# Kernel tuning notes

Hardware: AMD Instinct MI355X
Metric: run time of the kernel (lower is better)

Reference implementation:

```python
import jax, jax.numpy as jnp
import numpy as np

NSITES = 64   # 2 * nphysical spin-orbital sites
BOND = 128    # MPS bond dimension D
BATCH = 16384 # sampled occupation configurations


def setup_inputs() -> dict:
    key = jax.random.key(0)
    k1, k2, k3, k4 = jax.random.split(key, 4)
    # Site tensors A[k, n] in R^{D x D}; scaled so chain products stay O(1).
    data = jax.random.normal(k1, (NSITES, 2, BOND, BOND), dtype=jnp.float32) / jnp.sqrt(jnp.float32(BOND))
    left = jax.random.normal(k2, (BOND,), dtype=jnp.float32)
    right = jax.random.normal(k3, (BOND,), dtype=jnp.float32)
    # Occupation-number vectors (0/1 per spin orbital).
    onstate = jax.random.randint(k4, (BATCH, NSITES), 0, 2, dtype=jnp.int32)
    # Orbital-ordering permutation (identity here).
    image2 = jnp.arange(NSITES, dtype=jnp.int32)
    return {"onstate": onstate, "data": data, "left": left, "right": right, "image2": image2}


def reference(onstate, data, left, right, image2):
    # Reorder physical indices per the stored orbital image: [B, NSITES]
    occ = onstate[:, image2]
    B = occ.shape[0]
    D = left.shape[0]
    v0 = jnp.broadcast_to(left, (B, D))  # left boundary, batched

    def step(v, xs):
        A, n = xs  # A: [2, D, D] site tensor, n: [B] occupations at this site
        # Contract with both quantum-number blocks, then select per sample
        # (equivalent to gathering the block indexed by the occupation).
        v_new = jnp.where((n == 1)[:, None], v @ A[1], v @ A[0])  # [B, D]
        return v_new, None

    vT, _ = jax.lax.scan(step, v0, (data, occ.T))
    return vT @ right  # amplitudes psi(n): [B]
```

## Files before the change

kernel.cpp:

```cpp
#include <hip/hip_runtime.h>
#include <hip/hip_bf16.h>

#define NS 64
#define NP 32
#define DIM 128
#define BATCH_N 16384

typedef float f32x4 __attribute__((ext_vector_type(4)));
typedef _Float16 f16x8 __attribute__((ext_vector_type(8)));
typedef unsigned int u32;
typedef unsigned long long u64;

__device__ __forceinline__ unsigned short f2h(float f) {
    _Float16 h = (_Float16)f;
    return __builtin_bit_cast(unsigned short, h);
}

__global__ __launch_bounds__(256)
void prep_pair_frags(const float* __restrict__ data,
                     unsigned short* __restrict__ afrag) {
    __shared__ float LA[2 * 32 * 129];
    __shared__ float LB[2 * 32 * 128];

    const int p   = blockIdx.x >> 2;
    const int kk  = blockIdx.x & 3;
    const int tid = threadIdx.x;
    const int kgrp = tid >> 5;
    const int mgrp = tid & 31;

    const float* A0 = data + ((size_t)(2 * p) * 2 + 0) * DIM * DIM;
    const float* A1 = A0 + DIM * DIM;
    const float* B0 = data + ((size_t)(2 * p + 1) * 2 + 0) * DIM * DIM;
    const float* B1 = B0 + DIM * DIM;

    for (int c = tid; c < 32 * DIM; c += 256) {
        int kl = c >> 7, j = c & 127;
        float a0 = A0[(kk * 32 + kl) * DIM + j];
        float a1 = A1[(kk * 32 + kl) * DIM + j];
        LA[kl * 129 + j] = a0;
        LA[32 * 129 + kl * 129 + j] = a1 - a0;
    }

    float acc[2][2][4][4];
#pragma unroll
    for (int L = 0; L < 2; ++L)
#pragma unroll
        for (int R = 0; R < 2; ++R)
#pragma unroll
            for (int i = 0; i < 4; ++i)
#pragma unroll
                for (int mi = 0; mi < 4; ++mi) acc[L][R][i][mi] = 0.f;

    for (int ch = 0; ch < 4; ++ch) {
        __syncthreads();
        for (int c = tid; c < 32 * DIM; c += 256) {
            int jl = c >> 7, m = c & 127;
            float b0 = B0[(ch * 32 + jl) * DIM + m];
            float b1 = B1[(ch * 32 + jl) * DIM + m];
            LB[jl * 128 + m] = b0;
            LB[4096 + jl * 128 + m] = b1 - b0;
        }
        __syncthreads();
#pragma unroll 2
        for (int jl = 0; jl < 32; ++jl) {
            int j = ch * 32 + jl;
            float la0[4], la1[4];
#pragma unroll
            for (int i = 0; i < 4; ++i) {
                la0[i] = LA[(kgrp * 4 + i) * 129 + j];
                la1[i] = LA[32 * 129 + (kgrp * 4 + i) * 129 + j];
            }
            f32x4 lb0 = *reinterpret_cast<const f32x4*>(&LB[jl * 128 + mgrp * 4]);
            f32x4 lb1 = *reinterpret_cast<const f32x4*>(&LB[4096 + jl * 128 + mgrp * 4]);
#pragma unroll
            for (int i = 0; i < 4; ++i)
#pragma unroll
                for (int mi = 0; mi < 4; ++mi) {
                    acc[0][0][i][mi] += la0[i] * lb0[mi];
                    acc[1][0][i][mi] += la1[i] * lb0[mi];
                    acc[0][1][i][mi] += la0[i] * lb1[mi];
                    acc[1][1][i][mi] += la1[i] * lb1[mi];
                }
        }
    }

#pragma unroll
    for (int t = 0; t < 4; ++t) {
        int L = t & 1, R = t >> 1;
#pragma unroll
        for (int i = 0; i < 4; ++i)
#pragma unroll
            for (int mi = 0; mi < 4; ++mi) {
                int k = kk * 32 + kgrp * 4 + i;
                int m = mgrp * 4 + mi;
                int g = (k & 31) >> 3, j = k & 7;
                int lane = g * 16 + (m & 15);
                int mm = m >> 4;
                size_t idx =
                    ((((((size_t)p * 4 + t) * 4 + kk) * 8 + mm) * 64 + lane) * 8) + j;
                afrag[idx] = f2h(acc[L][R][i][mi]);
            }
    }
}

__global__ void prep_bits(const int* __restrict__ onstate,
                          const int* __restrict__ image2,
                          u64* __restrict__ bits) {
    int r = blockIdx.x * blockDim.x + threadIdx.x;
    if (r >= BATCH_N) return;
    const int* row = onstate + (size_t)r * NS;
    u64 b = 0;
#pragma unroll 8
    for (int t = 0; t < NS; ++t) {
        b |= ((u64)(row[image2[t]] & 1)) << t;
    }
    bits[r] = b;
}

__global__ __launch_bounds__(512, 2)
void mps_pair(const unsigned short* __restrict__ afrag,
              const u64* __restrict__ occbits,
              const float* __restrict__ left,
              const float* __restrict__ right,
              float* __restrict__ out) {
    __shared__ unsigned short vlds[2][64 * DIM];
    __shared__ float red[64][33];

    const int tid  = threadIdx.x;
    const int wid  = tid >> 6;
    const int lane = tid & 63;
    const int li   = lane & 15;
    const int g    = lane >> 4;
    const int rbase = blockIdx.x * 64;

    u64 bits[4];
#pragma unroll
    for (int rg = 0; rg < 4; ++rg)
        bits[rg] = occbits[rbase + rg * 16 + li];

    u32 rdoff[4][4];
#pragma unroll
    for (int rg = 0; rg < 4; ++rg)
#pragma unroll
        for (int kk = 0; kk < 4; ++kk) {
            int r = rg * 16 + li;
            rdoff[rg][kk] =
                (u32)(r * 256 + kk * 64 + g * 16) ^ ((u32)(r & 7) << 4);
        }
    u32 wroff[4];
#pragma unroll
    for (int rg = 0; rg < 4; ++rg) {
        int r = rg * 16 + li;
        int mbase = wid * 16 + g * 4;
        wroff[rg] = (u32)(r * 256 + mbase * 2) ^ ((u32)(r & 7) << 4);
    }

    for (int c = tid; c < 64 * 16; c += 512) {
        int r  = c >> 4;
        int kc = c & 15;
        unsigned short tmp[8];
#pragma unroll
        for (int j = 0; j < 8; ++j) tmp[j] = f2h(left[kc * 8 + j]);
        u32 byte = (u32)(r * 256 + kc * 16) ^ ((u32)(r & 7) << 4);
        *reinterpret_cast<uint4*>(reinterpret_cast<char*>(&vlds[0][0]) + byte) =
            *reinterpret_cast<uint4*>(tmp);
    }
    __syncthreads();

    const f16x8 zf = {0, 0, 0, 0, 0, 0, 0, 0};

    f16x8 ft[2][4][4];

#define ISSUE(BUF, P_)                                                        \
    {                                                                         \
        const unsigned short* sb_ = afrag + (size_t)(P_) * 65536;             \
        _Pragma("unroll")                                                     \
        for (int t = 0; t < 4; ++t)                                           \
            _Pragma("unroll")                                                 \
            for (int kk = 0; kk < 4; ++kk)                                    \
                ft[BUF][t][kk] = *reinterpret_cast<const f16x8*>(             \
                    sb_ + ((size_t)((t * 4 + kk) * 8 + wid) * 512) +          \
                    lane * 8);                                                \
    }

#define COMPUTE(P_, BUF)                                                      \
    {                                                                         \
        const int p_ = (P_);                                                  \
        const char* vb = reinterpret_cast<const char*>(&vlds[p_ & 1][0]);     \
        char*       wb = reinterpret_cast<char*>(&vlds[(p_ + 1) & 1][0]);     \
        f32x4 acc[4];                                                         \
        _Pragma("unroll")                                                     \
        for (int rg = 0; rg < 4; ++rg) acc[rg] = (f32x4){0.f, 0.f, 0.f, 0.f}; \
        __builtin_amdgcn_s_setprio(1);                                        \
        _Pragma("unroll")                                                     \
        for (int kk = 0; kk < 4; ++kk) {                                      \
            f16x8 bfr[4];                                                     \
            _Pragma("unroll")                                                 \
            for (int rg = 0; rg < 4; ++rg)                                    \
                bfr[rg] =                                                     \
                    *reinterpret_cast<const f16x8*>(vb + rdoff[rg][kk]);      \
            _Pragma("unroll")                                                 \
            for (int rg = 0; rg < 4; ++rg) {                                  \
                bool m0 = (bits[rg] >> (2 * p_)) & 1;                         \
                bool m1 = (bits[rg] >> (2 * p_ + 1)) & 1;                     \
                f16x8 vb0  = m0 ? bfr[rg] : zf;                               \
                f16x8 vb1  = m1 ? bfr[rg] : zf;                               \
                f16x8 vb01 = m1 ? vb0 : zf;                                   \
                acc[rg] = __builtin_amdgcn_mfma_f32_16x16x32_f16(             \
                    ft[BUF][0][kk], bfr[rg], acc[rg], 0, 0, 0);               \
                acc[rg] = __builtin_amdgcn_mfma_f32_16x16x32_f16(             \
                    ft[BUF][1][kk], vb0, acc[rg], 0, 0, 0);                   \
                acc[rg] = __builtin_amdgcn_mfma_f32_16x16x32_f16(             \
                    ft[BUF][2][kk], vb1, acc[rg], 0, 0, 0);                   \
                acc[rg] = __builtin_amdgcn_mfma_f32_16x16x32_f16(             \
                    ft[BUF][3][kk], vb01, acc[rg], 0, 0, 0);                  \
            }                                                                 \
        }                                                                     \
        __builtin_amdgcn_s_setprio(0);                                        \
        if (p_ < NP - 1) {                                                    \
            _Pragma("unroll")                                                 \
            for (int rg = 0; rg < 4; ++rg) {                                  \
                u32 lo = ((u32)f2h(acc[rg][1]) << 16) | f2h(acc[rg][0]);      \
                u32 hi = ((u32)f2h(acc[rg][3]) << 16) | f2h(acc[rg][2]);      \
                uint2 w = {lo, hi};                                           \
                *reinterpret_cast<uint2*>(wb + wroff[rg]) = w;                \
            }                                                                 \
            __syncthreads();                                                  \
        } else {                                                              \
            int mcol = wid * 16 + g * 4;                                      \
            const float4 rv = *reinterpret_cast<const float4*>(right + mcol); \
            _Pragma("unroll")                                                 \
            for (int rg = 0; rg < 4; ++rg) {                                  \
                float pv = acc[rg][0] * rv.x + acc[rg][1] * rv.y +            \
                           acc[rg][2] * rv.z + acc[rg][3] * rv.w;             \
                red[rg * 16 + li][wid * 4 + g] = pv;                          \
            }                                                                 \
            __syncthreads();                                                  \
            if (tid < 64) {                                                   \
                float ssum = 0.f;                                             \
                _Pragma("unroll")                                             \
                for (int i = 0; i < 32; ++i) ssum += red[tid][i];             \
                out[rbase + tid] = ssum;                                      \
            }                                                                 \
        }                                                                     \
    }

    ISSUE(0, 0);
    for (int pp = 0; pp < NP; pp += 2) {
        ISSUE(1, pp + 1);
        COMPUTE(pp, 0);
        if (pp + 2 < NP) ISSUE(0, pp + 2);
        COMPUTE(pp + 1, 1);
    }

#undef ISSUE
#undef COMPUTE
}

extern "C" void kernel_launch(void* const* d_in, const int* in_sizes, int n_in,
                              void* d_out, int out_size, void* d_ws, size_t ws_size,
                              hipStream_t stream) {
    const int*   onstate = (const int*)d_in[0];
    const float* data    = (const float*)d_in[1];
    const float* left    = (const float*)d_in[2];
    const float* right   = (const float*)d_in[3];
    const int*   image2  = (const int*)d_in[4];
    float* out = (float*)d_out;

    unsigned short* afrag = (unsigned short*)d_ws;
    u64* bits = (u64*)((char*)d_ws + (size_t)2097152 * sizeof(unsigned short));

    prep_pair_frags<<<128, 256, 0, stream>>>(data, afrag);
    prep_bits<<<64, 256, 0, stream>>>(onstate, image2, bits);
    mps_pair<<<256, 512, 0, stream>>>(afrag, bits, left, right, out);
}
```

Baseline: 113.4 us.

## Halve rows per block and split fragment prefetch into half-K chunks

The main kernel now processes 32 batch rows per block instead of 64, launching 512 blocks, and raises the occupancy hint from 2 to 4 blocks per CU. The A-fragment register double-buffer is restructured from whole-pair buffers into two half-K chunks, so the next pair's first half loads while the current second half computes. This cuts register and LDS use per block to allow more resident waves and fill all CUs. In exchange, every block reloads the same site fragments for fewer rows, doubling global/L2 fragment traffic per row, and the prefetch distance is shorter.

```diff
diff --git a/kernel.cpp b/kernel.cpp
--- a/kernel.cpp
+++ b/kernel.cpp
@@ -117,47 +117,47 @@
     bits[r] = b;
 }
 
-__global__ __launch_bounds__(512, 2)
+__global__ __launch_bounds__(512, 4)
 void mps_pair(const unsigned short* __restrict__ afrag,
               const u64* __restrict__ occbits,
               const float* __restrict__ left,
               const float* __restrict__ right,
               float* __restrict__ out) {
-    __shared__ unsigned short vlds[2][64 * DIM];
-    __shared__ float red[64][33];
+    __shared__ unsigned short vlds[2][32 * DIM];
+    __shared__ float red[32][33];
 
     const int tid  = threadIdx.x;
     const int wid  = tid >> 6;
     const int lane = tid & 63;
     const int li   = lane & 15;
     const int g    = lane >> 4;
-    const int rbase = blockIdx.x * 64;
-
-    u64 bits[4];
-#pragma unroll
-    for (int rg = 0; rg < 4; ++rg)
+    const int rbase = blockIdx.x * 32;
+
+    u64 bits[2];
+#pragma unroll
+    for (int rg = 0; rg < 2; ++rg)
         bits[rg] = occbits[rbase + rg * 16 + li];
 
-    u32 rdoff[4][4];
-#pragma unroll
-    for (int rg = 0; rg < 4; ++rg)
+    u32 rdoff[2][4];
+#pragma unroll
+    for (int rg = 0; rg < 2; ++rg)
 #pragma unroll
         for (int kk = 0; kk < 4; ++kk) {
             int r = rg * 16 + li;
             rdoff[rg][kk] =
                 (u32)(r * 256 + kk * 64 + g * 16) ^ ((u32)(r & 7) << 4);
         }
-    u32 wroff[4];
-#pragma unroll
-    for (int rg = 0; rg < 4; ++rg) {
+    u32 wroff[2];
+#pragma unroll
+    for (int rg = 0; rg < 2; ++rg) {
         int r = rg * 16 + li;
         int mbase = wid * 16 + g * 4;
         wroff[rg] = (u32)(r * 256 + mbase * 2) ^ ((u32)(r & 7) << 4);
     }
 
-    for (int c = tid; c < 64 * 16; c += 512) {
-        int r  = c >> 4;
-        int kc = c & 15;
+    if (tid < 32 * 16) {
+        int r  = tid >> 4;
+        int kc = tid & 15;
         unsigned short tmp[8];
 #pragma unroll
         for (int j = 0; j < 8; ++j) tmp[j] = f2h(left[kc * 8 + j]);
@@ -169,57 +169,60 @@
 
     const f16x8 zf = {0, 0, 0, 0, 0, 0, 0, 0};
 
-    f16x8 ft[2][4][4];
-
-#define ISSUE(BUF, P_)                                                        \
+    f16x8 ft0[4][2], ft1[4][2];
+    f32x4 acc[2];
+
+#define ISSUE_CHUNK(FT, P_, H_)                                               \
     {                                                                         \
         const unsigned short* sb_ = afrag + (size_t)(P_) * 65536;             \
         _Pragma("unroll")                                                     \
         for (int t = 0; t < 4; ++t)                                           \
             _Pragma("unroll")                                                 \
-            for (int kk = 0; kk < 4; ++kk)                                    \
-                ft[BUF][t][kk] = *reinterpret_cast<const f16x8*>(             \
-                    sb_ + ((size_t)((t * 4 + kk) * 8 + wid) * 512) +          \
+            for (int kq = 0; kq < 2; ++kq)                                    \
+                FT[t][kq] = *reinterpret_cast<const f16x8*>(                  \
+                    sb_ +                                                     \
+                    ((size_t)((t * 4 + 2 * (H_) + kq) * 8 + wid) * 512) +     \
                     lane * 8);                                                \
     }
 
-#define COMPUTE(P_, BUF)                                                      \
+#define COMPUTE_HALF(P_, H_, FT)                                              \
     {                                                                         \
         const int p_ = (P_);                                                  \
         const char* vb = reinterpret_cast<const char*>(&vlds[p_ & 1][0]);     \
-        char*       wb = reinterpret_cast<char*>(&vlds[(p_ + 1) & 1][0]);     \
-        f32x4 acc[4];                                                         \
         _Pragma("unroll")                                                     \
-        for (int rg = 0; rg < 4; ++rg) acc[rg] = (f32x4){0.f, 0.f, 0.f, 0.f}; \
-        __builtin_amdgcn_s_setprio(1);                                        \
-        _Pragma("unroll")                                                     \
-        for (int kk = 0; kk < 4; ++kk) {                                      \
-            f16x8 bfr[4];                                                     \
-            _Pragma("unroll")                                                 \
-            for (int rg = 0; rg < 4; ++rg)                                    \
+        for (int kq = 0; kq < 2; ++kq) {                                      \
+            const int kk = 2 * (H_) + kq;                                     \
+            f16x8 bfr[2];                                                     \
+            _Pragma("unroll")                                                 \
+            for (int rg = 0; rg < 2; ++rg)                                    \
                 bfr[rg] =                                                     \
                     *reinterpret_cast<const f16x8*>(vb + rdoff[rg][kk]);      \
             _Pragma("unroll")                                                 \
-            for (int rg = 0; rg < 4; ++rg) {                                  \
+            for (int rg = 0; rg < 2; ++rg) {                                  \
                 bool m0 = (bits[rg] >> (2 * p_)) & 1;                         \
                 bool m1 = (bits[rg] >> (2 * p_ + 1)) & 1;                     \
                 f16x8 vb0  = m0 ? bfr[rg] : zf;                               \
                 f16x8 vb1  = m1 ? bfr[rg] : zf;                               \
                 f16x8 vb01 = m1 ? vb0 : zf;                                   \
                 acc[rg] = __builtin_amdgcn_mfma_f32_16x16x32_f16(             \
-                    ft[BUF][0][kk], bfr[rg], acc[rg], 0, 0, 0);               \
-                acc[rg] = __builtin_amdgcn_mfma_f32_16x16x32_f16(             \
-                    ft[BUF][1][kk], vb0, acc[rg], 0, 0, 0);                   \
-                acc[rg] = __builtin_amdgcn_mfma_f32_16x16x32_f16(             \
-                    ft[BUF][2][kk], vb1, acc[rg], 0, 0, 0);                   \
-                acc[rg] = __builtin_amdgcn_mfma_f32_16x16x32_f16(             \
-                    ft[BUF][3][kk], vb01, acc[rg], 0, 0, 0);                  \
+                    FT[0][kq], bfr[rg], acc[rg], 0, 0, 0);                    \
+                acc[rg] = __builtin_amdgcn_mfma_f32_16x16x32_f16(             \
+                    FT[1][kq], vb0, acc[rg], 0, 0, 0);                        \
+                acc[rg] = __builtin_amdgcn_mfma_f32_16x16x32_f16(             \
+                    FT[2][kq], vb1, acc[rg], 0, 0, 0);                        \
+                acc[rg] = __builtin_amdgcn_mfma_f32_16x16x32_f16(             \
+                    FT[3][kq], vb01, acc[rg], 0, 0, 0);                       \
             }                                                                 \
         }                                                                     \
-        __builtin_amdgcn_s_setprio(0);                                        \
+    }
+
+#define WRITE_PHASE(P_)                                                       \
+    {                                                                         \
+        const int p_ = (P_);                                                  \
+        char* wb = reinterpret_cast<char*>(&vlds[(p_ + 1) & 1][0]);           \
         if (p_ < NP - 1) {                                                    \
             _Pragma("unroll")                                                 \
-            for (int rg = 0; rg < 4; ++rg) {                                  \
+            for (int rg = 0; rg < 2; ++rg) {                                  \
                 u32 lo = ((u32)f2h(acc[rg][1]) << 16) | f2h(acc[rg][0]);      \
                 u32 hi = ((u32)f2h(acc[rg][3]) << 16) | f2h(acc[rg][2]);      \
                 uint2 w = {lo, hi};                                           \
@@ -230,13 +233,13 @@
             int mcol = wid * 16 + g * 4;                                      \
             const float4 rv = *reinterpret_cast<const float4*>(right + mcol); \
             _Pragma("unroll")                                                 \
-            for (int rg = 0; rg < 4; ++rg) {                                  \
+            for (int rg = 0; rg < 2; ++rg) {                                  \
                 float pv = acc[rg][0] * rv.x + acc[rg][1] * rv.y +            \
                            acc[rg][2] * rv.z + acc[rg][3] * rv.w;             \
                 red[rg * 16 + li][wid * 4 + g] = pv;                          \
             }                                                                 \
             __syncthreads();                                                  \
-            if (tid < 64) {                                                   \
+            if (tid < 32) {                                                   \
                 float ssum = 0.f;                                             \
                 _Pragma("unroll")                                             \
                 for (int i = 0; i < 32; ++i) ssum += red[tid][i];             \
@@ -245,16 +248,20 @@
         }                                                                     \
     }
 
-    ISSUE(0, 0);
-    for (int pp = 0; pp < NP; pp += 2) {
-        ISSUE(1, pp + 1);
-        COMPUTE(pp, 0);
-        if (pp + 2 < NP) ISSUE(0, pp + 2);
-        COMPUTE(pp + 1, 1);
-    }
-
-#undef ISSUE
-#undef COMPUTE
+    ISSUE_CHUNK(ft0, 0, 0);
+    for (int p = 0; p < NP; ++p) {
+        acc[0] = (f32x4){0.f, 0.f, 0.f, 0.f};
+        acc[1] = (f32x4){0.f, 0.f, 0.f, 0.f};
+        ISSUE_CHUNK(ft1, p, 1);
+        COMPUTE_HALF(p, 0, ft0);
+        if (p + 1 < NP) ISSUE_CHUNK(ft0, p + 1, 0);
+        COMPUTE_HALF(p, 1, ft1);
+        WRITE_PHASE(p);
+    }
+
+#undef ISSUE_CHUNK
+#undef COMPUTE_HALF
+#undef WRITE_PHASE
 }
 
 extern "C" void kernel_launch(void* const* d_in, const int* in_sizes, int n_in,
@@ -272,5 +279,5 @@
 
     prep_pair_frags<<<128, 256, 0, stream>>>(data, afrag);
     prep_bits<<<64, 256, 0, stream>>>(onstate, image2, bits);
-    mps_pair<<<256, 512, 0, stream>>>(afrag, bits, left, right, out);
-}
+    mps_pair<<<512, 512, 0, stream>>>(afrag, bits, left, right, out);
+}
```

New measurement: 126.9 us. 1.12x slower.
